# Performance work log

Measured on AMD Instinct MI355X. Metric: run time of the kernel, lower is better.

Reference implementation:

```python
import jax, jax.numpy as jnp
import numpy as np

# Tree layout: NUM_LEVELS topological levels, M nodes per level; children of a node in
# level l are drawn from levels < l (level-0 nodes are leaves). This batches all
# independent same-level nodes, exactly the structure the per-node python loop implies.
NUM_LEVELS = 16
N_NODES = 16384
M_PER_LEVEL = N_NODES // NUM_LEVELS  # 1024
K_CHILD = 4
D_IN = 1024
D_HID = 256


def _linear_params(key, fan_in, fan_out):
    kw, kb = jax.random.split(key)
    bound = 1.0 / np.sqrt(fan_in)
    W = jax.random.uniform(kw, (fan_out, fan_in), jnp.float32, -bound, bound)
    b = jax.random.uniform(kb, (fan_out,), jnp.float32, -bound, bound)
    return W, b


def setup_inputs() -> dict:
    key = jax.random.key(0)
    kx, k1, k2, k3, k4 = jax.random.split(key, 5)
    x = jax.random.normal(kx, (N_NODES, D_IN), dtype=jnp.float32)

    # children: [N, K] int32, -1 = no child; child indices lie in strictly lower levels
    rng = np.random.default_rng(0)
    level = np.arange(N_NODES) // M_PER_LEVEL  # [N]
    lo_count = np.maximum(level * M_PER_LEVEL, 1)  # nodes available below each node
    cand = (rng.random((N_NODES, K_CHILD)) * lo_count[:, None]).astype(np.int64)
    present = (rng.random((N_NODES, K_CHILD)) < 0.6) & (level[:, None] > 0)
    children = jnp.asarray(np.where(present, cand, -1), dtype=jnp.int32)

    Wioux, bioux = _linear_params(k1, D_IN, 3 * D_HID)
    Wiouh, biouh = _linear_params(k2, D_HID, 3 * D_HID)
    Wfx, bfx = _linear_params(k3, D_IN, D_HID)
    Wfh, bfh = _linear_params(k4, D_HID, D_HID)
    return {"x": x, "children": children,
            "Wioux": Wioux, "bioux": bioux, "Wiouh": Wiouh, "biouh": biouh,
            "Wfx": Wfx, "bfx": bfx, "Wfh": Wfh, "bfh": bfh}


def reference(x, children, Wioux, bioux, Wiouh, biouh, Wfx, bfx, Wfh, bfh):
    N, _ = x.shape
    H = Wfh.shape[0]
    K = children.shape[1]
    L = NUM_LEVELS
    M = N // L

    # Input-dependent gate pre-activations: one big GEMM for all nodes (ioux / fx)
    iou_x = (x @ Wioux.T + bioux).reshape(L, M, 3 * H)
    f_x = (x @ Wfx.T + bfx).reshape(L, M, H)
    ch = jnp.maximum(children, 0).reshape(L, M, K)
    mk = (children >= 0).astype(x.dtype).reshape(L, M, K)

    def step(carry, inp):
        h, c = carry  # [N, H] each
        l, iou_xl, f_xl, chl, ml = inp
        h_ch = h[chl] * ml[..., None]  # [M, K, H] gathered child hidden states
        c_ch = c[chl] * ml[..., None]  # [M, K, H]
        # child-sum TreeLSTM: i/o/u gates use sum of child hidden states
        iou = iou_xl + h_ch.sum(axis=1) @ Wiouh.T + biouh  # [M, 3H]
        ig, og, ug = jnp.split(iou, 3, axis=-1)
        ig, og, ug = jax.nn.sigmoid(ig), jax.nn.sigmoid(og), jnp.tanh(ug)
        # per-child forget gates
        f = jax.nn.sigmoid(f_xl[:, None, :] + h_ch @ Wfh.T + bfh)  # [M, K, H]
        cl = ig * ug + jnp.sum(f * c_ch, axis=1)  # [M, H]
        hl = og * jnp.tanh(cl)
        h = jax.lax.dynamic_update_slice(h, hl, (l * M, 0))
        c = jax.lax.dynamic_update_slice(c, cl, (l * M, 0))
        return (h, c), None

    init = (jnp.zeros((N, H), x.dtype), jnp.zeros((N, H), x.dtype))
    xs = (jnp.arange(L, dtype=jnp.int32), iou_x, f_x, ch, mk)
    (h, _), _ = jax.lax.scan(step, init, xs)
    return h  # [N, H] hidden state of every node
```

## Files before the change

kernel.cpp:

```cpp
#include <hip/hip_runtime.h>
#include <stdint.h>

typedef __attribute__((ext_vector_type(8))) short bf16x8;
typedef __attribute__((ext_vector_type(4))) float f32x4;
typedef __attribute__((ext_vector_type(4))) unsigned int u32x4;
typedef unsigned short u16;
typedef unsigned int u32;

#define NLVL 16
#define NNODE 16384
#define DIN 1024
#define DH 256

__device__ __forceinline__ u16 f2bf(float f) {
  u32 u = __builtin_bit_cast(u32, f);
  u += 0x7FFFu + ((u >> 16) & 1u);
  return (u16)(u >> 16);
}
__device__ __forceinline__ float b2f(u16 h) {
  u32 u = ((u32)h) << 16;
  return __builtin_bit_cast(float, u);
}
__device__ __forceinline__ float fsig(float x) {
  return __builtin_amdgcn_rcpf(1.0f + __expf(-x));
}
__device__ __forceinline__ float ftanh(float x) {
  return 1.0f - 2.0f * __builtin_amdgcn_rcpf(__expf(2.0f * x) + 1.0f);
}

__device__ __forceinline__ void async_copy16(const void* g, void* lds) {
  __builtin_amdgcn_global_load_lds((const __attribute__((address_space(1))) void*)g,
                                   (__attribute__((address_space(3))) void*)lds, 16, 0, 0);
}

__device__ __forceinline__ void gload_x4(u32x4& v, const void* p) {
  asm volatile("global_load_dwordx4 %0, %1, off sc0 sc1" : "=&v"(v) : "v"(p));
}
__device__ __forceinline__ void gstore_dw(float* p, float v) {
  asm volatile("global_store_dword %0, %1, off sc0 sc1" :: "v"(p), "v"(v) : "memory");
}
__device__ __forceinline__ void gstore_sh(u16* p, u16 v) {
  u32 w = v;
  asm volatile("global_store_short %0, %1, off sc0 sc1" :: "v"(p), "v"(w) : "memory");
}
__device__ __forceinline__ float aload_f(const float* p) {
  u32 v = __hip_atomic_load((const u32*)p, __ATOMIC_RELAXED, __HIP_MEMORY_SCOPE_AGENT);
  return __builtin_bit_cast(float, v);
}

__global__ __launch_bounds__(256) void k_prep(
    const float* __restrict__ x,
    const float* __restrict__ Wioux, const float* __restrict__ Wfx,
    const float* __restrict__ Wiouh, const float* __restrict__ Wfh,
    const float* __restrict__ bioux, const float* __restrict__ bfx,
    const float* __restrict__ biouh, const float* __restrict__ bfh,
    u16* __restrict__ xb, u16* __restrict__ Wxb, u16* __restrict__ Whb,
    float* __restrict__ b1, float* __restrict__ b2) {
  if (blockIdx.x < 8192) {
    size_t i = (size_t)blockIdx.x * 256 + threadIdx.x;
    const float4* p = (const float4*)x + i * 2;
    float4 v0 = p[0], v1 = p[1];
    union { u16 s[8]; uint4 v; } o;
    o.s[0] = f2bf(v0.x); o.s[1] = f2bf(v0.y); o.s[2] = f2bf(v0.z); o.s[3] = f2bf(v0.w);
    o.s[4] = f2bf(v1.x); o.s[5] = f2bf(v1.y); o.s[6] = f2bf(v1.z); o.s[7] = f2bf(v1.w);
    *((uint4*)(xb + i * 8)) = o.v;
    return;
  }
  int t = (blockIdx.x - 8192) * 256 + threadIdx.x;
  if (t < 131072) {
    int idx = t * 8;
    int row = idx >> 10, col = idx & 1023;
    const float* src = (row < 768) ? (Wioux + (size_t)row * 1024 + col)
                                   : (Wfx + (size_t)(row - 768) * 1024 + col);
    union { u16 s[8]; uint4 v; } o;
#pragma unroll
    for (int j = 0; j < 8; ++j) o.s[j] = f2bf(src[j]);
    *((uint4*)(Wxb + idx)) = o.v;
  } else if (t < 163840) {
    int idx = (t - 131072) * 8;
    int row = idx >> 8, col = idx & 255;
    const float* src = (row < 768) ? (Wiouh + (size_t)row * 256 + col)
                                   : (Wfh + (size_t)(row - 768) * 256 + col);
    union { u16 s[8]; uint4 v; } o;
#pragma unroll
    for (int j = 0; j < 8; ++j) o.s[j] = f2bf(src[j]);
    *((uint4*)(Whb + idx)) = o.v;
  } else if (t < 164096) {
    int idx = (t - 163840) * 8;
#pragma unroll
    for (int j = 0; j < 8; ++j) {
      int i = idx + j;
      if (i < 1024) b1[i] = (i < 768) ? bioux[i] : bfx[i - 768];
      else { int k = i - 1024; b2[k] = (k < 768) ? biouh[k] : bfh[k - 768]; }
    }
  }
}

__device__ __forceinline__ int swz2(int row) { return (row & 3) ^ ((row >> 2) & 3); }

__global__ __launch_bounds__(256) void k_fused(
    const u16* __restrict__ xb, const int* __restrict__ children,
    const u16* __restrict__ Wxb, const u16* __restrict__ Whb,
    const float* __restrict__ b1, const float* __restrict__ b2,
    float* __restrict__ gx, u16* __restrict__ hb, float* __restrict__ cb,
    float* __restrict__ hout, u32* __restrict__ flags, u32* __restrict__ gxflag) {
  __shared__ __align__(16) char smem[71168];
  const int tid = threadIdx.x, w = tid >> 6, l = tid & 63;
  const int bid = blockIdx.x;

  if (bid < 256) {
    u16* As = (u16*)smem;
    u16* Bs = (u16*)(smem + 16384);
    const int wm = w >> 1, wn = w & 1;
    for (int r = 0; r < 4; ++r) {
      const int job = bid + r * 256;
      const int level = job >> 6, sub = job & 63;
      const int tM = level * 1024 + (sub >> 3) * 128, tN = (sub & 7) * 128;

      f32x4 acc[4][4];
#pragma unroll
      for (int mt = 0; mt < 4; ++mt)
#pragma unroll
        for (int nt = 0; nt < 4; ++nt) acc[mt][nt] = (f32x4){0.f, 0.f, 0.f, 0.f};

      auto stage = [&](int buf, int t) {
        int k0 = t * 32;
#pragma unroll
        for (int i = 0; i < 2; ++i) {
          int seg = w * 2 + i;
          int row = seg * 16 + (l >> 2);
          int qg = (l & 3) ^ swz2(row);
          async_copy16(xb + (size_t)(tM + row) * 1024 + k0 + qg * 8,
                       &As[buf * 4096 + seg * 512]);
          async_copy16(Wxb + (size_t)(tN + row) * 1024 + k0 + qg * 8,
                       &Bs[buf * 4096 + seg * 512]);
        }
      };
      auto compute = [&](int buf) {
        bf16x8 a[4], b[4];
#pragma unroll
        for (int mt = 0; mt < 4; ++mt) {
          int row = wm * 64 + mt * 16 + (l & 15);
          int cs = (l >> 4) ^ swz2(row);
          a[mt] = *(const bf16x8*)&As[buf * 4096 + row * 32 + cs * 8];
        }
#pragma unroll
        for (int nt = 0; nt < 4; ++nt) {
          int row = wn * 64 + nt * 16 + (l & 15);
          int cs = (l >> 4) ^ swz2(row);
          b[nt] = *(const bf16x8*)&Bs[buf * 4096 + row * 32 + cs * 8];
        }
#pragma unroll
        for (int mt = 0; mt < 4; ++mt)
#pragma unroll
          for (int nt = 0; nt < 4; ++nt)
            acc[mt][nt] = __builtin_amdgcn_mfma_f32_16x16x32_bf16(a[mt], b[nt], acc[mt][nt], 0, 0, 0);
      };

      stage(0, 0);
      __syncthreads();
      int buf = 0;
      for (int t = 0; t < 32; ++t) {
        if (t + 1 < 32) stage(buf ^ 1, t + 1);
        compute(buf);
        __syncthreads();
        buf ^= 1;
      }

#pragma unroll
      for (int mt = 0; mt < 4; ++mt)
#pragma unroll
        for (int nt = 0; nt < 4; ++nt) {
          int col = tN + wn * 64 + nt * 16 + (l & 15);
          float bias = b1[col];
          int rbase = tM + wm * 64 + mt * 16 + (l >> 4) * 4;
#pragma unroll
          for (int rr = 0; rr < 4; ++rr)
            gstore_dw(gx + (size_t)(rbase + rr) * 1024 + col, acc[mt][nt][rr] + bias);
        }
      asm volatile("s_waitcnt vmcnt(0)" ::: "memory");
      __syncthreads();
      if (tid == 0)
        __hip_atomic_fetch_add(gxflag + level, 1u, __ATOMIC_RELAXED, __HIP_MEMORY_SCOPE_AGENT);
      __syncthreads();
    }
    return;
  }

  int* ch = (int*)smem;
  u16* hch = (u16*)(smem + 256);
  u16* hsum = (u16*)(smem + 33024);
  float* c_lds = (float*)(smem + 41216);
  float* iouA = (float*)(smem + 58624);
  const int lb = bid - 256;
  const int ntile = lb & 63;
  const int h0 = (lb >> 6) * 64;

  bf16x8 w1[3][8];
  int colg_[3]; float b1g_[3];
#pragma unroll
  for (int i = 0; i < 3; ++i) {
    int tt = w * 3 + i;
    int s = tt >> 2, t = tt & 3;
    int colg = s * 256 + h0 + t * 16 + (l & 15);
    colg_[i] = colg;
    b1g_[i] = b2[colg];
    const u16* bp = Whb + (size_t)colg * 256 + (l >> 4) * 8;
#pragma unroll
    for (int ks = 0; ks < 8; ++ks) w1[i][ks] = *(const bf16x8*)(bp + ks * 32);
  }
  bf16x8 w2[4][8];
  float b2g_[4];
#pragma unroll
  for (int nt = 0; nt < 4; ++nt) {
    int hcol = h0 + nt * 16 + (l & 15);
    b2g_[nt] = b2[768 + hcol];
    const u16* bp = Whb + (size_t)(768 + hcol) * 256 + (l >> 4) * 8;
#pragma unroll
    for (int ks = 0; ks < 8; ++ks) w2[nt][ks] = *(const bf16x8*)(bp + ks * 32);
  }

  for (int level = 0; level < NLVL; ++level) {
    const int node0 = level * 1024 + ntile * 16;
    if (tid < 64) ch[tid] = children[node0 * 4 + tid];
    __syncthreads();

    if (level > 0 && tid < 64) {
      int child = ch[tid];
      if (child >= 0) {
        const u32* f = flags + (child >> 4);
        while (__hip_atomic_load(f, __ATOMIC_RELAXED, __HIP_MEMORY_SCOPE_AGENT) < 4u)
          __builtin_amdgcn_s_sleep(4);
      }
    }
    __syncthreads();

    u32x4 hv[8]; int hc[8];
#pragma unroll
    for (int it = 0; it < 8; ++it) {
      int id = tid + it * 256;
      int row = id >> 5, q = id & 31;
      int child = ch[row]; hc[it] = child;
      int cr = child < 0 ? 0 : child;
      gload_x4(hv[it], hb + (size_t)cr * 256 + q * 8);
    }
    u32x4 cv[4]; int cc[4];
#pragma unroll
    for (int it = 0; it < 4; ++it) {
      int id = tid + it * 256;
      int row = id >> 4, qq = id & 15;
      int child = ch[row]; cc[it] = child;
      int cr = child < 0 ? 0 : child;
      gload_x4(cv[it], cb + (size_t)cr * 256 + h0 + qq * 4);
    }
    asm volatile("s_waitcnt vmcnt(0)"
                 : "+v"(hv[0]), "+v"(hv[1]), "+v"(hv[2]), "+v"(hv[3]),
                   "+v"(hv[4]), "+v"(hv[5]), "+v"(hv[6]), "+v"(hv[7]),
                   "+v"(cv[0]), "+v"(cv[1]), "+v"(cv[2]), "+v"(cv[3]) :: "memory");
    __builtin_amdgcn_sched_barrier(0);
#pragma unroll
    for (int it = 0; it < 8; ++it) {
      int id = tid + it * 256;
      int row = id >> 5, q = id & 31;
      u32x4 v = hv[it];
      if (hc[it] < 0) v = (u32x4){0u, 0u, 0u, 0u};
      *(u32x4*)&hch[row * 256 + ((q ^ (row & 7)) * 8)] = v;
    }
#pragma unroll
    for (int it = 0; it < 4; ++it) {
      int id = tid + it * 256;
      int row = id >> 4, qq = id & 15;
      u32x4 v = cv[it];
      if (cc[it] < 0) v = (u32x4){0u, 0u, 0u, 0u};
      *(u32x4*)&c_lds[row * 68 + qq * 4] = v;
    }
    __syncthreads();

#pragma unroll
    for (int it = 0; it < 2; ++it) {
      int id = tid + it * 256;
      int row = id >> 5, q = id & 31;
      float s[8] = {0.f, 0.f, 0.f, 0.f, 0.f, 0.f, 0.f, 0.f};
#pragma unroll
      for (int k = 0; k < 4; ++k) {
        int hr = row * 4 + k;
        bf16x8 v = *(const bf16x8*)&hch[hr * 256 + ((q ^ (hr & 7)) * 8)];
#pragma unroll
        for (int j = 0; j < 8; ++j) s[j] += b2f((u16)v[j]);
      }
      union { u16 us[8]; u32x4 v4; } o;
#pragma unroll
      for (int j = 0; j < 8; ++j) o.us[j] = f2bf(s[j]);
      *(u32x4*)&hsum[row * 256 + ((q ^ (row & 7)) * 8)] = o.v4;
    }
    if (tid == 0) {
      while (__hip_atomic_load(gxflag + level, __ATOMIC_RELAXED, __HIP_MEMORY_SCOPE_AGENT) < 64u)
        __builtin_amdgcn_s_sleep(2);
    }
    __syncthreads();

    float gxv[3][4], fxv[4];
#pragma unroll
    for (int i = 0; i < 3; ++i)
#pragma unroll
      for (int r = 0; r < 4; ++r)
        gxv[i][r] = aload_f(gx + (size_t)(node0 + (l >> 4) * 4 + r) * 1024 + colg_[i]);
    {
      const int node = node0 + w * 4 + (l >> 4);
#pragma unroll
      for (int nt = 0; nt < 4; ++nt)
        fxv[nt] = aload_f(gx + (size_t)node * 1024 + 768 + h0 + nt * 16 + (l & 15));
    }

    bf16x8 a1[8];
    {
      int arow = l & 15;
#pragma unroll
      for (int ks = 0; ks < 8; ++ks) {
        int chunk = ks * 4 + (l >> 4);
        a1[ks] = *(const bf16x8*)&hsum[arow * 256 + ((chunk ^ (arow & 7)) * 8)];
      }
    }
#pragma unroll
    for (int i = 0; i < 3; ++i) {
      int tt = w * 3 + i;
      int s = tt >> 2, t = tt & 3;
      f32x4 acc = (f32x4){0.f, 0.f, 0.f, 0.f};
#pragma unroll
      for (int ks = 0; ks < 8; ++ks)
        acc = __builtin_amdgcn_mfma_f32_16x16x32_bf16(a1[ks], w1[i][ks], acc, 0, 0, 0);
      float bias = b1g_[i];
#pragma unroll
      for (int r = 0; r < 4; ++r) {
        int nodeL = (l >> 4) * 4 + r;
        float v = acc[r] + gxv[i][r] + bias;
        iouA[nodeL * 196 + s * 64 + t * 16 + (l & 15)] = (s < 2) ? fsig(v) : ftanh(v);
      }
    }
    __syncthreads();

    bf16x8 a2[8];
    {
      int arow = w * 16 + (l & 15);
#pragma unroll
      for (int ks = 0; ks < 8; ++ks) {
        int chunk = ks * 4 + (l >> 4);
        a2[ks] = *(const bf16x8*)&hch[arow * 256 + ((chunk ^ (arow & 7)) * 8)];
      }
    }
    const int nodeL = w * 4 + (l >> 4);
    const int node = node0 + nodeL;
#pragma unroll
    for (int nt = 0; nt < 4; ++nt) {
      int hl = nt * 16 + (l & 15);
      int hcol = h0 + hl;
      f32x4 acc = (f32x4){0.f, 0.f, 0.f, 0.f};
#pragma unroll
      for (int ks = 0; ks < 8; ++ks)
        acc = __builtin_amdgcn_mfma_f32_16x16x32_bf16(a2[ks], w2[nt][ks], acc, 0, 0, 0);
      float fx = fxv[nt] + b2g_[nt];
      float fcsum = 0.f;
#pragma unroll
      for (int r = 0; r < 4; ++r)
        fcsum += fsig(fx + acc[r]) * c_lds[(nodeL * 4 + r) * 68 + hl];
      float ig = iouA[nodeL * 196 + hl];
      float og = iouA[nodeL * 196 + 64 + hl];
      float ug = iouA[nodeL * 196 + 128 + hl];
      float cnew = ig * ug + fcsum;
      float hnew = og * ftanh(cnew);
      hout[(size_t)node * 256 + hcol] = hnew;
      gstore_dw(cb + (size_t)node * 256 + hcol, cnew);
      gstore_sh(hb + (size_t)node * 256 + hcol, f2bf(hnew));
    }
    asm volatile("s_waitcnt vmcnt(0)" ::: "memory");
    __syncthreads();
    if (tid == 0)
      __hip_atomic_fetch_add(flags + ((level << 6) + ntile), 1u,
                             __ATOMIC_RELAXED, __HIP_MEMORY_SCOPE_AGENT);
  }
}

extern "C" void kernel_launch(void* const* d_in, const int* in_sizes, int n_in,
                              void* d_out, int out_size, void* d_ws, size_t ws_size,
                              hipStream_t stream) {
  const float* x = (const float*)d_in[0];
  const int* children = (const int*)d_in[1];
  const float* Wioux = (const float*)d_in[2];
  const float* bioux = (const float*)d_in[3];
  const float* Wiouh = (const float*)d_in[4];
  const float* biouh = (const float*)d_in[5];
  const float* Wfx = (const float*)d_in[6];
  const float* bfx = (const float*)d_in[7];
  const float* Wfh = (const float*)d_in[8];
  const float* bfh = (const float*)d_in[9];

  char* ws = (char*)d_ws;
  u16* xb = (u16*)(ws + 0);
  float* gx = (float*)(ws + 33554432);
  u16* hb = (u16*)(ws + 100663296);
  float* cb = (float*)(ws + 109051904);
  u16* Wxb = (u16*)(ws + 125829120);
  u16* Whb = (u16*)(ws + 127926272);
  float* b1 = (float*)(ws + 128450560);
  float* b2 = (float*)(ws + 128454656);
  u32* flags = (u32*)(ws + 128458752);
  u32* gxflag = (u32*)(ws + 128462848);
  float* hout = (float*)d_out;

  hipMemsetAsync(flags, 0, 8192, stream);
  k_prep<<<8833, 256, 0, stream>>>(x, Wioux, Wfx, Wiouh, Wfh, bioux, bfx, biouh, bfh,
                                   xb, Wxb, Whb, b1, b2);
  k_fused<<<512, 256, 0, stream>>>(xb, children, Wxb, Whb, b1, b2,
                                   gx, hb, cb, hout, flags, gxflag);
}
```

Measured before the change: 250.0 us.

## Split child waits by level, per-colgroup flags, preload children, early gx loads

Preloads all 16 levels of child indices into LDS once instead of per level. Replaces the counting flag per node tile with four per-column-group flags read as one vector load. Loads from children in older levels are issued right away, and only children in the immediately previous level are waited on and loaded afterward, so the gather overlaps with the dependency wait. The gx wait and loads move earlier, and the final level skips the h/c stores and flag publish. The price is more LDS, a larger flag buffer and more complex synchronisation logic.

New measurement: 209.5 us. 16.2% less time.

```diff
diff --git a/kernel.cpp b/kernel.cpp
--- a/kernel.cpp
+++ b/kernel.cpp
@@ -35,6 +35,12 @@
 
 __device__ __forceinline__ void gload_x4(u32x4& v, const void* p) {
   asm volatile("global_load_dwordx4 %0, %1, off sc0 sc1" : "=&v"(v) : "v"(p));
+}
+__device__ __forceinline__ u32x4 gload_x4_sync(const void* p) {
+  u32x4 v;
+  asm volatile("global_load_dwordx4 %0, %1, off sc0 sc1\n\ts_waitcnt vmcnt(0)"
+               : "=&v"(v) : "v"(p) : "memory");
+  return v;
 }
 __device__ __forceinline__ void gstore_dw(float* p, float v) {
   asm volatile("global_store_dword %0, %1, off sc0 sc1" :: "v"(p), "v"(v) : "memory");
@@ -104,7 +110,7 @@
     const float* __restrict__ b1, const float* __restrict__ b2,
     float* __restrict__ gx, u16* __restrict__ hb, float* __restrict__ cb,
     float* __restrict__ hout, u32* __restrict__ flags, u32* __restrict__ gxflag) {
-  __shared__ __align__(16) char smem[71168];
+  __shared__ __align__(16) char smem[75264];
   const int tid = threadIdx.x, w = tid >> 6, l = tid & 63;
   const int bid = blockIdx.x;
 
@@ -187,14 +193,15 @@
     return;
   }
 
-  int* ch = (int*)smem;
-  u16* hch = (u16*)(smem + 256);
-  u16* hsum = (u16*)(smem + 33024);
-  float* c_lds = (float*)(smem + 41216);
-  float* iouA = (float*)(smem + 58624);
+  int* chAll = (int*)smem;
+  u16* hch = (u16*)(smem + 4096);
+  u16* hsum = (u16*)(smem + 36864);
+  float* c_lds = (float*)(smem + 45056);
+  float* iouA = (float*)(smem + 62464);
   const int lb = bid - 256;
   const int ntile = lb & 63;
-  const int h0 = (lb >> 6) * 64;
+  const int cg = lb >> 6;
+  const int h0 = cg * 64;
 
   bf16x8 w1[3][8];
   int colg_[3]; float b1g_[3];
@@ -220,18 +227,32 @@
     for (int ks = 0; ks < 8; ++ks) w2[nt][ks] = *(const bf16x8*)(bp + ks * 32);
   }
 
+#pragma unroll
+  for (int k = 0; k < 4; ++k) {
+    int id = tid + k * 256;
+    chAll[id] = children[(size_t)(id >> 6) * 4096 + ntile * 64 + (id & 63)];
+  }
+  __syncthreads();
+
   for (int level = 0; level < NLVL; ++level) {
     const int node0 = level * 1024 + ntile * 16;
-    if (tid < 64) ch[tid] = children[node0 * 4 + tid];
-    __syncthreads();
+    const int* ch = chAll + level * 64;
+    const int thr = (level - 1) << 10;
 
     if (level > 0 && tid < 64) {
       int child = ch[tid];
-      if (child >= 0) {
-        const u32* f = flags + (child >> 4);
-        while (__hip_atomic_load(f, __ATOMIC_RELAXED, __HIP_MEMORY_SCOPE_AGENT) < 4u)
-          __builtin_amdgcn_s_sleep(4);
-      }
+      if (child >= 0 && child < thr) {
+        const u32* fp = flags + (size_t)(child >> 4) * 4;
+        for (;;) {
+          u32x4 fv = gload_x4_sync(fp);
+          if ((fv[0] & fv[1] & fv[2] & fv[3]) != 0u) break;
+          __builtin_amdgcn_s_sleep(2);
+        }
+      }
+    }
+    if (tid == 0) {
+      while (__hip_atomic_load(gxflag + level, __ATOMIC_RELAXED, __HIP_MEMORY_SCOPE_AGENT) < 64u)
+        __builtin_amdgcn_s_sleep(2);
     }
     __syncthreads();
 
@@ -241,8 +262,9 @@
       int id = tid + it * 256;
       int row = id >> 5, q = id & 31;
       int child = ch[row]; hc[it] = child;
-      int cr = child < 0 ? 0 : child;
-      gload_x4(hv[it], hb + (size_t)cr * 256 + q * 8);
+      hv[it] = (u32x4){0u, 0u, 0u, 0u};
+      if (child >= 0 && child < thr)
+        gload_x4(hv[it], hb + (size_t)child * 256 + q * 8);
     }
     u32x4 cv[4]; int cc[4];
 #pragma unroll
@@ -250,9 +272,41 @@
       int id = tid + it * 256;
       int row = id >> 4, qq = id & 15;
       int child = ch[row]; cc[it] = child;
-      int cr = child < 0 ? 0 : child;
-      gload_x4(cv[it], cb + (size_t)cr * 256 + h0 + qq * 4);
-    }
+      cv[it] = (u32x4){0u, 0u, 0u, 0u};
+      if (child >= 0 && child < thr)
+        gload_x4(cv[it], cb + (size_t)child * 256 + h0 + qq * 4);
+    }
+
+    if (level > 0) {
+      if (tid < 64) {
+        int child = ch[tid];
+        if (child >= thr) {
+          const u32* fp = flags + (size_t)(child >> 4) * 4;
+          for (;;) {
+            u32x4 fv = gload_x4_sync(fp);
+            if ((fv[0] & fv[1] & fv[2] & fv[3]) != 0u) break;
+            __builtin_amdgcn_s_sleep(2);
+          }
+        }
+      }
+      __syncthreads();
+
+#pragma unroll
+      for (int it = 0; it < 8; ++it) {
+        int id = tid + it * 256;
+        int row = id >> 5, q = id & 31;
+        if (hc[it] >= thr)
+          gload_x4(hv[it], hb + (size_t)hc[it] * 256 + q * 8);
+      }
+#pragma unroll
+      for (int it = 0; it < 4; ++it) {
+        int id = tid + it * 256;
+        int row = id >> 4, qq = id & 15;
+        if (cc[it] >= thr)
+          gload_x4(cv[it], cb + (size_t)cc[it] * 256 + h0 + qq * 4);
+      }
+    }
+
     asm volatile("s_waitcnt vmcnt(0)"
                  : "+v"(hv[0]), "+v"(hv[1]), "+v"(hv[2]), "+v"(hv[3]),
                    "+v"(hv[4]), "+v"(hv[5]), "+v"(hv[6]), "+v"(hv[7]),
@@ -262,20 +316,28 @@
     for (int it = 0; it < 8; ++it) {
       int id = tid + it * 256;
       int row = id >> 5, q = id & 31;
-      u32x4 v = hv[it];
-      if (hc[it] < 0) v = (u32x4){0u, 0u, 0u, 0u};
-      *(u32x4*)&hch[row * 256 + ((q ^ (row & 7)) * 8)] = v;
+      *(u32x4*)&hch[row * 256 + ((q ^ (row & 7)) * 8)] = hv[it];
     }
 #pragma unroll
     for (int it = 0; it < 4; ++it) {
       int id = tid + it * 256;
       int row = id >> 4, qq = id & 15;
-      u32x4 v = cv[it];
-      if (cc[it] < 0) v = (u32x4){0u, 0u, 0u, 0u};
-      *(u32x4*)&c_lds[row * 68 + qq * 4] = v;
+      *(u32x4*)&c_lds[row * 68 + qq * 4] = cv[it];
     }
     __syncthreads();
 
+    float gxv[3][4], fxv[4];
+#pragma unroll
+    for (int i = 0; i < 3; ++i)
+#pragma unroll
+      for (int r = 0; r < 4; ++r)
+        gxv[i][r] = aload_f(gx + (size_t)(node0 + (l >> 4) * 4 + r) * 1024 + colg_[i]);
+    {
+      const int node = node0 + w * 4 + (l >> 4);
+#pragma unroll
+      for (int nt = 0; nt < 4; ++nt)
+        fxv[nt] = aload_f(gx + (size_t)node * 1024 + 768 + h0 + nt * 16 + (l & 15));
+    }
 #pragma unroll
     for (int it = 0; it < 2; ++it) {
       int id = tid + it * 256;
@@ -293,24 +355,7 @@
       for (int j = 0; j < 8; ++j) o.us[j] = f2bf(s[j]);
       *(u32x4*)&hsum[row * 256 + ((q ^ (row & 7)) * 8)] = o.v4;
     }
-    if (tid == 0) {
-      while (__hip_atomic_load(gxflag + level, __ATOMIC_RELAXED, __HIP_MEMORY_SCOPE_AGENT) < 64u)
-        __builtin_amdgcn_s_sleep(2);
-    }
     __syncthreads();
-
-    float gxv[3][4], fxv[4];
-#pragma unroll
-    for (int i = 0; i < 3; ++i)
-#pragma unroll
-      for (int r = 0; r < 4; ++r)
-        gxv[i][r] = aload_f(gx + (size_t)(node0 + (l >> 4) * 4 + r) * 1024 + colg_[i]);
-    {
-      const int node = node0 + w * 4 + (l >> 4);
-#pragma unroll
-      for (int nt = 0; nt < 4; ++nt)
-        fxv[nt] = aload_f(gx + (size_t)node * 1024 + 768 + h0 + nt * 16 + (l & 15));
-    }
 
     bf16x8 a1[8];
     {
@@ -369,14 +414,18 @@
       float cnew = ig * ug + fcsum;
       float hnew = og * ftanh(cnew);
       hout[(size_t)node * 256 + hcol] = hnew;
-      gstore_dw(cb + (size_t)node * 256 + hcol, cnew);
-      gstore_sh(hb + (size_t)node * 256 + hcol, f2bf(hnew));
-    }
-    asm volatile("s_waitcnt vmcnt(0)" ::: "memory");
-    __syncthreads();
-    if (tid == 0)
-      __hip_atomic_fetch_add(flags + ((level << 6) + ntile), 1u,
-                             __ATOMIC_RELAXED, __HIP_MEMORY_SCOPE_AGENT);
+      if (level + 1 < NLVL) {
+        gstore_dw(cb + (size_t)node * 256 + hcol, cnew);
+        gstore_sh(hb + (size_t)node * 256 + hcol, f2bf(hnew));
+      }
+    }
+    if (level + 1 < NLVL) {
+      asm volatile("s_waitcnt vmcnt(0)" ::: "memory");
+      __syncthreads();
+      if (tid == 0)
+        __hip_atomic_store(flags + (size_t)((level << 6) + ntile) * 4 + cg, 1u,
+                           __ATOMIC_RELAXED, __HIP_MEMORY_SCOPE_AGENT);
+    }
   }
 }
 
@@ -404,10 +453,10 @@
   float* b1 = (float*)(ws + 128450560);
   float* b2 = (float*)(ws + 128454656);
   u32* flags = (u32*)(ws + 128458752);
-  u32* gxflag = (u32*)(ws + 128462848);
+  u32* gxflag = (u32*)(ws + 128475136);
   float* hout = (float*)d_out;
 
-  hipMemsetAsync(flags, 0, 8192, stream);
+  hipMemsetAsync(flags, 0, 20480, stream);
   k_prep<<<8833, 256, 0, stream>>>(x, Wioux, Wfx, Wiouh, Wfh, bioux, bfx, biouh, bfh,
                                    xb, Wxb, Whb, b1, b2);
   k_fused<<<512, 256, 0, stream>>>(xb, children, Wxb, Whb, b1, b2,
```
